# Optimization experiments

Hardware: AMD Instinct MI355X
Metric: run time of the kernel (lower is better)

The kernel has to match this reference:

```python
import jax, jax.numpy as jnp
import numpy as np

N, M, IN_DIM, OUT_DIM = 32768, 8192, 256, 64


def setup_inputs() -> dict:
    key = jax.random.key(0)
    k1, k2, k3, k4 = jax.random.split(key, 4)
    H = jax.random.bernoulli(k1, 0.01, (N, M)).astype(jnp.float32)
    w = jax.random.uniform(k2, (M,), minval=0.5, maxval=1.5, dtype=jnp.float32)
    x = jax.random.normal(k3, (N, IN_DIM), dtype=jnp.float32)
    W_lin = jax.random.normal(k4, (IN_DIM, OUT_DIM), dtype=jnp.float32) * (1.0 / np.sqrt(IN_DIM))
    b_lin = jnp.zeros((OUT_DIM,), dtype=jnp.float32)
    return {"x": x, "H": H, "w": w, "W_lin": W_lin, "b_lin": b_lin}


def reference(x, H, w, W_lin, b_lin):
    # Theta = Dv^{-1/2} H diag(w) De^{-1} H^T Dv^{-1/2}; out = Theta @ (x W + b).
    # Applied right-to-left with O(N) diagonal broadcasts instead of materializing
    # the [N, N] operator -- identical math to the torch reference.
    De = jnp.clip(jnp.sum(H, axis=0), 1.0, None)                 # [M] edge degrees
    Dv = jnp.clip(jnp.sum(H * w[None, :], axis=1), 1e-6, None)   # [N] weighted node degrees
    dv_inv_sqrt = Dv ** -0.5                                     # [N]
    y = x @ W_lin + b_lin                                        # [N, out]
    t = H.T @ (dv_inv_sqrt[:, None] * y)                         # [M, out] gather to edges
    t = (w / De)[:, None] * t                                    # edge scaling W De^{-1}
    out = dv_inv_sqrt[:, None] * (H @ t)                         # [N, out] scatter back
    return out
```

## Files before the change

kernel.cpp:

```cpp
#include <hip/hip_runtime.h>

#define N_NODES 32768
#define M_EDGES 8192
#define IN_DIM  256
#define OUT_F   64

#define SCAN_ROWS 16
#define NBLK   (N_NODES / SCAN_ROWS)
#define RBCAP  192
#define COLCAP 512

__global__ __launch_bounds__(256) void k_scan(const float* __restrict__ H,
                                              const float* __restrict__ w,
                                              unsigned short* __restrict__ rowidx,
                                              unsigned* __restrict__ rowlen,
                                              unsigned short* __restrict__ cscidx,
                                              unsigned* __restrict__ cscfill,
                                              float* __restrict__ Dv_raw) {
    int tid  = threadIdx.x;
    int lane = tid & 63;
    int wid  = tid >> 6;
    int row0 = blockIdx.x * SCAN_ROWS;

    for (int rr = wid; rr < SCAN_ROWS; rr += 4) {
        int n = row0 + rr;
        const float4* Hrow = (const float4*)(H + (size_t)n * M_EDGES);
        unsigned short* out_r = rowidx + (size_t)n * RBCAP;

        unsigned mreg[4];
        #pragma unroll
        for (int ob = 0; ob < 4; ++ob) {
            int jb = ob * 512;
            float4 h0 = Hrow[jb + lane];
            float4 h1 = Hrow[jb + 64  + lane];
            float4 h2 = Hrow[jb + 128 + lane];
            float4 h3 = Hrow[jb + 192 + lane];
            float4 h4 = Hrow[jb + 256 + lane];
            float4 h5 = Hrow[jb + 320 + lane];
            float4 h6 = Hrow[jb + 384 + lane];
            float4 h7 = Hrow[jb + 448 + lane];
            unsigned mk = 0;
            #define PK(hv, g)                                                  \
            {                                                                  \
                unsigned b = (unsigned)(hv.x != 0.f)                           \
                           | ((unsigned)(hv.y != 0.f) << 1)                    \
                           | ((unsigned)(hv.z != 0.f) << 2)                    \
                           | ((unsigned)(hv.w != 0.f) << 3);                   \
                mk |= b << (4 * (g));                                          \
            }
            PK(h0, 0) PK(h1, 1) PK(h2, 2) PK(h3, 3)
            PK(h4, 4) PK(h5, 5) PK(h6, 6) PK(h7, 7)
            #undef PK
            mreg[ob] = mk;
        }

        unsigned cnt = (unsigned)(__popc(mreg[0]) + __popc(mreg[1])
                                + __popc(mreg[2]) + __popc(mreg[3]));
        unsigned incl = cnt;
        #pragma unroll
        for (int off = 1; off < 64; off <<= 1) {
            unsigned v = (unsigned)__shfl_up((int)incl, off, 64);
            if (lane >= off) incl += v;
        }
        unsigned pos = incl - cnt;
        unsigned total = (unsigned)__shfl((int)incl, 63, 64);

        float dv = 0.f;
        #pragma unroll
        for (int r = 0; r < 4; ++r) {
            unsigned mm = mreg[r];
            while (mm) {
                int p = __ffs(mm) - 1;
                int g = p >> 2;
                int c4 = p & 3;
                int m_idx = r * 2048 + g * 256 + (lane << 2) + c4;
                if (pos < RBCAP) out_r[pos] = (unsigned short)m_idx;
                ++pos;
                dv += w[m_idx];
                unsigned fp = atomicAdd(&cscfill[m_idx], 1u);
                if (fp < (unsigned)COLCAP)
                    cscidx[(size_t)m_idx * COLCAP + fp] = (unsigned short)n;
                mm &= mm - 1;
            }
        }
        for (int off = 32; off; off >>= 1) dv += __shfl_down(dv, off, 64);
        if (lane == 0) Dv_raw[n] = dv;
        if (lane == 63)
            rowlen[n] = (total < (unsigned)RBCAP) ? total : (unsigned)RBCAP;
    }
}

__global__ __launch_bounds__(256) void k_lin(const float* __restrict__ x,
                                             const float* __restrict__ Wl,
                                             const float* __restrict__ b,
                                             const float* __restrict__ Dv_raw,
                                             float* __restrict__ y2) {
    __shared__ float x_s[16 * IN_DIM];
    int tid = threadIdx.x;
    int n0 = blockIdx.x * 16;
    for (int i = tid; i < 16 * IN_DIM; i += 256)
        x_s[i] = x[(size_t)n0 * IN_DIM + i];
    __syncthreads();
    int k = tid & 63;
    int rbase = tid >> 6;
    for (int pass = 0; pass < 4; ++pass) {
        int r = pass * 4 + rbase;
        float acc = b[k];
        const float* xr = x_s + r * IN_DIM;
        #pragma unroll 8
        for (int i = 0; i < IN_DIM; ++i)
            acc = fmaf(xr[i], Wl[i * OUT_F + k], acc);
        float dvis = rsqrtf(fmaxf(Dv_raw[n0 + r], 1e-6f));
        y2[(size_t)(n0 + r) * OUT_F + k] = acc * dvis;
    }
}

#define SEGQ(vi, base, cnt, src, ax, ay, az, aw, g, c, lane)                   \
if ((base) < (cnt)) {                                                          \
    unsigned rem = (cnt) - (base); if (rem > 64u) rem = 64u;                   \
    unsigned nq = (rem + 3u) >> 2;                                             \
    _Pragma("unroll 4")                                                        \
    for (unsigned qq = 0; qq < nq; ++qq) {                                     \
        int nidx = __shfl(vi, (int)(4u * qq) + (g), 64);                       \
        const float4* srcp = (const float4*)((src) + (size_t)nidx * OUT_F);    \
        float4 v = srcp[c];                                                    \
        bool ok = (4u * qq + (unsigned)(g)) < rem;                             \
        ax += ok ? v.x : 0.f;                                                  \
        ay += ok ? v.y : 0.f;                                                  \
        az += ok ? v.z : 0.f;                                                  \
        aw += ok ? v.w : 0.f;                                                  \
    }                                                                          \
}

__global__ __launch_bounds__(256) void k_edge(const unsigned short* __restrict__ cscidx,
                                              const unsigned* __restrict__ cscfill,
                                              const float* __restrict__ w,
                                              const float* __restrict__ y2,
                                              float* __restrict__ t) {
    int lane = threadIdx.x & 63;
    int wid  = threadIdx.x >> 6;
    int m = blockIdx.x * 4 + wid;
    unsigned de = cscfill[m];
    unsigned cnt = (de < (unsigned)COLCAP) ? de : (unsigned)COLCAP;
    const unsigned short* cp = cscidx + (size_t)m * COLCAP;
    int g = lane >> 4;
    int c = lane & 15;
    int v0 = cp[lane];         int v1 = cp[64  + lane];
    int v2 = cp[128 + lane];   int v3 = cp[192 + lane];
    int v4 = cp[256 + lane];   int v5 = cp[320 + lane];
    int v6 = cp[384 + lane];   int v7 = cp[448 + lane];
    float ax = 0.f, ay = 0.f, az = 0.f, aw = 0.f;
    SEGQ(v0,   0u, cnt, y2, ax, ay, az, aw, g, c, lane)
    SEGQ(v1,  64u, cnt, y2, ax, ay, az, aw, g, c, lane)
    SEGQ(v2, 128u, cnt, y2, ax, ay, az, aw, g, c, lane)
    SEGQ(v3, 192u, cnt, y2, ax, ay, az, aw, g, c, lane)
    SEGQ(v4, 256u, cnt, y2, ax, ay, az, aw, g, c, lane)
    SEGQ(v5, 320u, cnt, y2, ax, ay, az, aw, g, c, lane)
    SEGQ(v6, 384u, cnt, y2, ax, ay, az, aw, g, c, lane)
    SEGQ(v7, 448u, cnt, y2, ax, ay, az, aw, g, c, lane)
    ax += __shfl_xor(ax, 16, 64); ax += __shfl_xor(ax, 32, 64);
    ay += __shfl_xor(ay, 16, 64); ay += __shfl_xor(ay, 32, 64);
    az += __shfl_xor(az, 16, 64); az += __shfl_xor(az, 32, 64);
    aw += __shfl_xor(aw, 16, 64); aw += __shfl_xor(aw, 32, 64);
    if (g == 0) {
        float sc = w[m] / fmaxf((float)de, 1.0f);
        float4 r4 = { ax * sc, ay * sc, az * sc, aw * sc };
        ((float4*)(t + (size_t)m * OUT_F))[c] = r4;
    }
}

__global__ __launch_bounds__(256) void k_out(const unsigned short* __restrict__ rowidx,
                                             const unsigned* __restrict__ rowlen,
                                             const float* __restrict__ t,
                                             const float* __restrict__ Dv_raw,
                                             float* __restrict__ out) {
    int lane = threadIdx.x & 63;
    int wid  = threadIdx.x >> 6;
    int n = blockIdx.x * 4 + wid;
    unsigned cnt = rowlen[n];
    const unsigned short* rp = rowidx + (size_t)n * RBCAP;
    int g = lane >> 4;
    int c = lane & 15;
    int v0 = rp[lane];
    int v1 = rp[64  + lane];
    int v2 = rp[128 + lane];
    float ax = 0.f, ay = 0.f, az = 0.f, aw = 0.f;
    SEGQ(v0,   0u, cnt, t, ax, ay, az, aw, g, c, lane)
    SEGQ(v1,  64u, cnt, t, ax, ay, az, aw, g, c, lane)
    SEGQ(v2, 128u, cnt, t, ax, ay, az, aw, g, c, lane)
    ax += __shfl_xor(ax, 16, 64); ax += __shfl_xor(ax, 32, 64);
    ay += __shfl_xor(ay, 16, 64); ay += __shfl_xor(ay, 32, 64);
    az += __shfl_xor(az, 16, 64); az += __shfl_xor(az, 32, 64);
    aw += __shfl_xor(aw, 16, 64); aw += __shfl_xor(aw, 32, 64);
    if (g == 0) {
        float dvis = rsqrtf(fmaxf(Dv_raw[n], 1e-6f));
        float4 r4 = { ax * dvis, ay * dvis, az * dvis, aw * dvis };
        ((float4*)(out + (size_t)n * OUT_F))[c] = r4;
    }
}

extern "C" void kernel_launch(void* const* d_in, const int* in_sizes, int n_in,
                              void* d_out, int out_size, void* d_ws, size_t ws_size,
                              hipStream_t stream) {
    const float* x  = (const float*)d_in[0];
    const float* H  = (const float*)d_in[1];
    const float* w  = (const float*)d_in[2];
    const float* Wl = (const float*)d_in[3];
    const float* bl = (const float*)d_in[4];
    float* out = (float*)d_out;

    float*    y2      = (float*)d_ws;
    float*    t       = y2 + (size_t)N_NODES * OUT_F;
    float*    Dv_raw  = t + (size_t)M_EDGES * OUT_F;
    unsigned* rowlen  = (unsigned*)(Dv_raw + N_NODES);
    unsigned* cscfill = rowlen + N_NODES;
    unsigned short* rowidx = (unsigned short*)(cscfill + M_EDGES);
    unsigned short* cscidx = rowidx + (size_t)N_NODES * RBCAP;

    hipMemsetAsync(cscfill, 0, M_EDGES * sizeof(unsigned), stream);

    k_scan<<<dim3(NBLK),         dim3(256), 0, stream>>>(H, w, rowidx, rowlen, cscidx, cscfill, Dv_raw);
    k_lin <<<dim3(N_NODES / 16), dim3(256), 0, stream>>>(x, Wl, bl, Dv_raw, y2);
    k_edge<<<dim3(M_EDGES / 4),  dim3(256), 0, stream>>>(cscidx, cscfill, w, y2, t);
    k_out <<<dim3(N_NODES / 4),  dim3(256), 0, stream>>>(rowidx, rowlen, t, Dv_raw, out);
}
```

Before: 1.549 ms.

## Split CSC build out of scan, stage weights in LDS, split edge gather across waves

Moves the CSC transpose construction (atomics and scattered 16-bit stores) out of the H-streaming scan kernel into a separate kernel that reads the compact row index lists. The scan now sums w from a shared-memory copy. k_lin stages W_lin in LDS and uses two accumulators. k_edge assigns one edge per block, with four waves each handling 128 incidences, and reduces their partials through shared memory. The intent is to keep the dominant H read bandwidth-bound without atomic stalls, at the cost of an extra launch, the 64 KB w and W_lin LDS tiles limiting occupancy, and more k_edge blocks.

```diff
diff --git a/kernel.cpp b/kernel.cpp
--- a/kernel.cpp
+++ b/kernel.cpp
@@ -14,13 +14,16 @@
                                               const float* __restrict__ w,
                                               unsigned short* __restrict__ rowidx,
                                               unsigned* __restrict__ rowlen,
-                                              unsigned short* __restrict__ cscidx,
-                                              unsigned* __restrict__ cscfill,
                                               float* __restrict__ Dv_raw) {
+    __shared__ float w_s[M_EDGES];
     int tid  = threadIdx.x;
     int lane = tid & 63;
     int wid  = tid >> 6;
     int row0 = blockIdx.x * SCAN_ROWS;
+
+    for (int i = tid; i < M_EDGES / 4; i += 256)
+        ((float4*)w_s)[i] = ((const float4*)w)[i];
+    __syncthreads();
 
     for (int rr = wid; rr < SCAN_ROWS; rr += 4) {
         int n = row0 + rr;
@@ -76,10 +79,7 @@
                 int m_idx = r * 2048 + g * 256 + (lane << 2) + c4;
                 if (pos < RBCAP) out_r[pos] = (unsigned short)m_idx;
                 ++pos;
-                dv += w[m_idx];
-                unsigned fp = atomicAdd(&cscfill[m_idx], 1u);
-                if (fp < (unsigned)COLCAP)
-                    cscidx[(size_t)m_idx * COLCAP + fp] = (unsigned short)n;
+                dv += w_s[m_idx];
                 mm &= mm - 1;
             }
         }
@@ -87,6 +87,27 @@
         if (lane == 0) Dv_raw[n] = dv;
         if (lane == 63)
             rowlen[n] = (total < (unsigned)RBCAP) ? total : (unsigned)RBCAP;
+    }
+}
+
+__global__ __launch_bounds__(256) void k_csc(const unsigned short* __restrict__ rowidx,
+                                             const unsigned* __restrict__ rowlen,
+                                             unsigned short* __restrict__ cscidx,
+                                             unsigned* __restrict__ cscfill) {
+    int lane = threadIdx.x & 63;
+    int wid  = threadIdx.x >> 6;
+    int n = blockIdx.x * 4 + wid;
+    unsigned cnt = rowlen[n];
+    const unsigned short* rp = rowidx + (size_t)n * RBCAP;
+    #pragma unroll
+    for (int s = 0; s < 3; ++s) {
+        unsigned idx = (unsigned)(s * 64 + lane);
+        if (idx < cnt) {
+            int m = rp[idx];
+            unsigned fp = atomicAdd(&cscfill[m], 1u);
+            if (fp < (unsigned)COLCAP)
+                cscidx[(size_t)m * COLCAP + fp] = (unsigned short)n;
+        }
     }
 }
 
@@ -96,22 +117,27 @@
                                              const float* __restrict__ Dv_raw,
                                              float* __restrict__ y2) {
     __shared__ float x_s[16 * IN_DIM];
+    __shared__ float w_sh[IN_DIM * OUT_F];
     int tid = threadIdx.x;
     int n0 = blockIdx.x * 16;
-    for (int i = tid; i < 16 * IN_DIM; i += 256)
-        x_s[i] = x[(size_t)n0 * IN_DIM + i];
+    for (int i = tid; i < 16 * IN_DIM / 4; i += 256)
+        ((float4*)x_s)[i] = ((const float4*)(x + (size_t)n0 * IN_DIM))[i];
+    for (int i = tid; i < IN_DIM * OUT_F / 4; i += 256)
+        ((float4*)w_sh)[i] = ((const float4*)Wl)[i];
     __syncthreads();
     int k = tid & 63;
     int rbase = tid >> 6;
     for (int pass = 0; pass < 4; ++pass) {
         int r = pass * 4 + rbase;
-        float acc = b[k];
+        float acc0 = b[k], acc1 = 0.f;
         const float* xr = x_s + r * IN_DIM;
         #pragma unroll 8
-        for (int i = 0; i < IN_DIM; ++i)
-            acc = fmaf(xr[i], Wl[i * OUT_F + k], acc);
+        for (int i = 0; i < IN_DIM; i += 2) {
+            acc0 = fmaf(xr[i],     w_sh[i * OUT_F + k],       acc0);
+            acc1 = fmaf(xr[i + 1], w_sh[(i + 1) * OUT_F + k], acc1);
+        }
         float dvis = rsqrtf(fmaxf(Dv_raw[n0 + r], 1e-6f));
-        y2[(size_t)(n0 + r) * OUT_F + k] = acc * dvis;
+        y2[(size_t)(n0 + r) * OUT_F + k] = (acc0 + acc1) * dvis;
     }
 }
 
@@ -137,35 +163,36 @@
                                               const float* __restrict__ w,
                                               const float* __restrict__ y2,
                                               float* __restrict__ t) {
+    __shared__ float4 part[4 * 16];
     int lane = threadIdx.x & 63;
     int wid  = threadIdx.x >> 6;
-    int m = blockIdx.x * 4 + wid;
+    int m = blockIdx.x;
     unsigned de = cscfill[m];
     unsigned cnt = (de < (unsigned)COLCAP) ? de : (unsigned)COLCAP;
     const unsigned short* cp = cscidx + (size_t)m * COLCAP;
     int g = lane >> 4;
     int c = lane & 15;
-    int v0 = cp[lane];         int v1 = cp[64  + lane];
-    int v2 = cp[128 + lane];   int v3 = cp[192 + lane];
-    int v4 = cp[256 + lane];   int v5 = cp[320 + lane];
-    int v6 = cp[384 + lane];   int v7 = cp[448 + lane];
+    unsigned b0 = 128u * (unsigned)wid;
+    int v0 = cp[b0 + lane];
+    int v1 = cp[b0 + 64u + lane];
     float ax = 0.f, ay = 0.f, az = 0.f, aw = 0.f;
-    SEGQ(v0,   0u, cnt, y2, ax, ay, az, aw, g, c, lane)
-    SEGQ(v1,  64u, cnt, y2, ax, ay, az, aw, g, c, lane)
-    SEGQ(v2, 128u, cnt, y2, ax, ay, az, aw, g, c, lane)
-    SEGQ(v3, 192u, cnt, y2, ax, ay, az, aw, g, c, lane)
-    SEGQ(v4, 256u, cnt, y2, ax, ay, az, aw, g, c, lane)
-    SEGQ(v5, 320u, cnt, y2, ax, ay, az, aw, g, c, lane)
-    SEGQ(v6, 384u, cnt, y2, ax, ay, az, aw, g, c, lane)
-    SEGQ(v7, 448u, cnt, y2, ax, ay, az, aw, g, c, lane)
+    SEGQ(v0, b0,       cnt, y2, ax, ay, az, aw, g, c, lane)
+    SEGQ(v1, b0 + 64u, cnt, y2, ax, ay, az, aw, g, c, lane)
     ax += __shfl_xor(ax, 16, 64); ax += __shfl_xor(ax, 32, 64);
     ay += __shfl_xor(ay, 16, 64); ay += __shfl_xor(ay, 32, 64);
     az += __shfl_xor(az, 16, 64); az += __shfl_xor(az, 32, 64);
     aw += __shfl_xor(aw, 16, 64); aw += __shfl_xor(aw, 32, 64);
-    if (g == 0) {
+    if (g == 0) part[wid * 16 + c] = make_float4(ax, ay, az, aw);
+    __syncthreads();
+    if (threadIdx.x < 16) {
+        int cc = threadIdx.x;
+        float4 p0 = part[cc], p1 = part[16 + cc], p2 = part[32 + cc], p3 = part[48 + cc];
         float sc = w[m] / fmaxf((float)de, 1.0f);
-        float4 r4 = { ax * sc, ay * sc, az * sc, aw * sc };
-        ((float4*)(t + (size_t)m * OUT_F))[c] = r4;
+        float4 r4 = { (p0.x + p1.x + p2.x + p3.x) * sc,
+                      (p0.y + p1.y + p2.y + p3.y) * sc,
+                      (p0.z + p1.z + p2.z + p3.z) * sc,
+                      (p0.w + p1.w + p2.w + p3.w) * sc };
+        ((float4*)(t + (size_t)m * OUT_F))[cc] = r4;
     }
 }
 
@@ -219,8 +246,9 @@
 
     hipMemsetAsync(cscfill, 0, M_EDGES * sizeof(unsigned), stream);
 
-    k_scan<<<dim3(NBLK),         dim3(256), 0, stream>>>(H, w, rowidx, rowlen, cscidx, cscfill, Dv_raw);
+    k_scan<<<dim3(NBLK),         dim3(256), 0, stream>>>(H, w, rowidx, rowlen, Dv_raw);
+    k_csc <<<dim3(N_NODES / 4),  dim3(256), 0, stream>>>(rowidx, rowlen, cscidx, cscfill);
     k_lin <<<dim3(N_NODES / 16), dim3(256), 0, stream>>>(x, Wl, bl, Dv_raw, y2);
-    k_edge<<<dim3(M_EDGES / 4),  dim3(256), 0, stream>>>(cscidx, cscfill, w, y2, t);
+    k_edge<<<dim3(M_EDGES),      dim3(256), 0, stream>>>(cscidx, cscfill, w, y2, t);
     k_out <<<dim3(N_NODES / 4),  dim3(256), 0, stream>>>(rowidx, rowlen, t, Dv_raw, out);
 }
```

New measurement: 1.630 ms. +5.2%, slower.

## Replace sparse gather/scatter with dense bf16 MFMA GEMMs over H

Applied to the files above, without the earlier changes.

Swaps the sparse CSR/CSC build and gather kernels for dense matrix multiplies on the matrix cores. H is transposed into a bf16 copy for the H^T·z product, and H is packed to bf16 in registers for the H·t product. Activations are split into hi and lo bf16 halves to keep close to fp32 accuracy. Split-K partial sums are reduced in separate kernels. This removes the atomics and irregular gathers, but it reads all of dense H twice, writes a 512MB transposed copy, and does about 100x more arithmetic than the sparse path.

```diff
diff --git a/kernel.cpp b/kernel.cpp
--- a/kernel.cpp
+++ b/kernel.cpp
@@ -5,101 +5,78 @@
 #define IN_DIM  256
 #define OUT_F   64
 
-#define SCAN_ROWS 16
-#define NBLK   (N_NODES / SCAN_ROWS)
-#define RBCAP  192
-#define COLCAP 512
-
-__global__ __launch_bounds__(256) void k_scan(const float* __restrict__ H,
+#define KC1 16
+#define KC2 4
+
+typedef __attribute__((ext_vector_type(8))) short  bf16x8;
+typedef __attribute__((ext_vector_type(4))) float  f32x4;
+
+__device__ __forceinline__ unsigned short f2bf_rne(float f) {
+    unsigned u = __float_as_uint(f);
+    unsigned r = (u + 0x7FFFu + ((u >> 16) & 1u)) >> 16;
+    return (unsigned short)r;
+}
+__device__ __forceinline__ float bf2f(unsigned short h) {
+    return __uint_as_float(((unsigned)h) << 16);
+}
+
+__global__ __launch_bounds__(256) void k_prep(const float* __restrict__ H,
                                               const float* __restrict__ w,
-                                              unsigned short* __restrict__ rowidx,
-                                              unsigned* __restrict__ rowlen,
-                                              unsigned short* __restrict__ cscidx,
-                                              unsigned* __restrict__ cscfill,
-                                              float* __restrict__ Dv_raw) {
-    int tid  = threadIdx.x;
-    int lane = tid & 63;
-    int wid  = tid >> 6;
-    int row0 = blockIdx.x * SCAN_ROWS;
-
-    for (int rr = wid; rr < SCAN_ROWS; rr += 4) {
-        int n = row0 + rr;
-        const float4* Hrow = (const float4*)(H + (size_t)n * M_EDGES);
-        unsigned short* out_r = rowidx + (size_t)n * RBCAP;
-
-        unsigned mreg[4];
-        #pragma unroll
-        for (int ob = 0; ob < 4; ++ob) {
-            int jb = ob * 512;
-            float4 h0 = Hrow[jb + lane];
-            float4 h1 = Hrow[jb + 64  + lane];
-            float4 h2 = Hrow[jb + 128 + lane];
-            float4 h3 = Hrow[jb + 192 + lane];
-            float4 h4 = Hrow[jb + 256 + lane];
-            float4 h5 = Hrow[jb + 320 + lane];
-            float4 h6 = Hrow[jb + 384 + lane];
-            float4 h7 = Hrow[jb + 448 + lane];
-            unsigned mk = 0;
-            #define PK(hv, g)                                                  \
-            {                                                                  \
-                unsigned b = (unsigned)(hv.x != 0.f)                           \
-                           | ((unsigned)(hv.y != 0.f) << 1)                    \
-                           | ((unsigned)(hv.z != 0.f) << 2)                    \
-                           | ((unsigned)(hv.w != 0.f) << 3);                   \
-                mk |= b << (4 * (g));                                          \
-            }
-            PK(h0, 0) PK(h1, 1) PK(h2, 2) PK(h3, 3)
-            PK(h4, 4) PK(h5, 5) PK(h6, 6) PK(h7, 7)
-            #undef PK
-            mreg[ob] = mk;
-        }
-
-        unsigned cnt = (unsigned)(__popc(mreg[0]) + __popc(mreg[1])
-                                + __popc(mreg[2]) + __popc(mreg[3]));
-        unsigned incl = cnt;
-        #pragma unroll
-        for (int off = 1; off < 64; off <<= 1) {
-            unsigned v = (unsigned)__shfl_up((int)incl, off, 64);
-            if (lane >= off) incl += v;
-        }
-        unsigned pos = incl - cnt;
-        unsigned total = (unsigned)__shfl((int)incl, 63, 64);
-
-        float dv = 0.f;
-        #pragma unroll
-        for (int r = 0; r < 4; ++r) {
-            unsigned mm = mreg[r];
-            while (mm) {
-                int p = __ffs(mm) - 1;
-                int g = p >> 2;
-                int c4 = p & 3;
-                int m_idx = r * 2048 + g * 256 + (lane << 2) + c4;
-                if (pos < RBCAP) out_r[pos] = (unsigned short)m_idx;
-                ++pos;
-                dv += w[m_idx];
-                unsigned fp = atomicAdd(&cscfill[m_idx], 1u);
-                if (fp < (unsigned)COLCAP)
-                    cscidx[(size_t)m_idx * COLCAP + fp] = (unsigned short)n;
-                mm &= mm - 1;
-            }
-        }
-        for (int off = 32; off; off >>= 1) dv += __shfl_down(dv, off, 64);
-        if (lane == 0) Dv_raw[n] = dv;
-        if (lane == 63)
-            rowlen[n] = (total < (unsigned)RBCAP) ? total : (unsigned)RBCAP;
+                                              unsigned short* __restrict__ HT,
+                                              float* __restrict__ Dv_raw,
+                                              float* __restrict__ De) {
+    __shared__ unsigned short ht_s[128][264];
+    __shared__ float w_s[128];
+    __shared__ float de_s[128];
+    int t = threadIdx.x;
+    int n0 = blockIdx.x * 256;
+    int m0 = blockIdx.y * 128;
+    if (t < 128) { w_s[t] = w[m0 + t]; de_s[t] = 0.f; }
+    __syncthreads();
+
+    int c  = t & 31;
+    int rp = t >> 5;
+    float de0 = 0.f, de1 = 0.f, de2 = 0.f, de3 = 0.f;
+    for (int it = 0; it < 32; ++it) {
+        int r = it * 8 + rp;
+        float4 hv = ((const float4*)(H + (size_t)(n0 + r) * M_EDGES + m0))[c];
+        int mb = 4 * c;
+        ht_s[mb + 0][r] = (unsigned short)(__float_as_uint(hv.x) >> 16);
+        ht_s[mb + 1][r] = (unsigned short)(__float_as_uint(hv.y) >> 16);
+        ht_s[mb + 2][r] = (unsigned short)(__float_as_uint(hv.z) >> 16);
+        ht_s[mb + 3][r] = (unsigned short)(__float_as_uint(hv.w) >> 16);
+        float dp = hv.x * w_s[mb] + hv.y * w_s[mb + 1]
+                 + hv.z * w_s[mb + 2] + hv.w * w_s[mb + 3];
+        dp += __shfl_xor(dp, 1, 64);  dp += __shfl_xor(dp, 2, 64);
+        dp += __shfl_xor(dp, 4, 64);  dp += __shfl_xor(dp, 8, 64);
+        dp += __shfl_xor(dp, 16, 64);
+        if ((t & 31) == 0) atomicAdd(&Dv_raw[n0 + r], dp);
+        de0 += hv.x; de1 += hv.y; de2 += hv.z; de3 += hv.w;
+    }
+    atomicAdd(&de_s[4 * c + 0], de0);
+    atomicAdd(&de_s[4 * c + 1], de1);
+    atomicAdd(&de_s[4 * c + 2], de2);
+    atomicAdd(&de_s[4 * c + 3], de3);
+    __syncthreads();
+    if (t < 128) atomicAdd(&De[m0 + t], de_s[t]);
+
+    int lane = t & 63, wv = t >> 6;
+    for (int i = 0; i < 32; ++i) {
+        int ml = wv * 32 + i;
+        ushort4 v = *(const ushort4*)&ht_s[ml][lane * 4];
+        *(ushort4*)(HT + (size_t)(m0 + ml) * N_NODES + n0 + lane * 4) = v;
     }
 }
 
 __global__ __launch_bounds__(256) void k_lin(const float* __restrict__ x,
                                              const float* __restrict__ Wl,
                                              const float* __restrict__ b,
-                                             const float* __restrict__ Dv_raw,
-                                             float* __restrict__ y2) {
+                                             float* __restrict__ y) {
     __shared__ float x_s[16 * IN_DIM];
     int tid = threadIdx.x;
     int n0 = blockIdx.x * 16;
-    for (int i = tid; i < 16 * IN_DIM; i += 256)
-        x_s[i] = x[(size_t)n0 * IN_DIM + i];
+    for (int i = tid; i < 16 * IN_DIM / 4; i += 256)
+        ((float4*)x_s)[i] = ((const float4*)(x + (size_t)n0 * IN_DIM))[i];
     __syncthreads();
     int k = tid & 63;
     int rbase = tid >> 6;
@@ -110,93 +87,205 @@
         #pragma unroll 8
         for (int i = 0; i < IN_DIM; ++i)
             acc = fmaf(xr[i], Wl[i * OUT_F + k], acc);
-        float dvis = rsqrtf(fmaxf(Dv_raw[n0 + r], 1e-6f));
-        y2[(size_t)(n0 + r) * OUT_F + k] = acc * dvis;
-    }
-}
-
-#define SEGQ(vi, base, cnt, src, ax, ay, az, aw, g, c, lane)                   \
-if ((base) < (cnt)) {                                                          \
-    unsigned rem = (cnt) - (base); if (rem > 64u) rem = 64u;                   \
-    unsigned nq = (rem + 3u) >> 2;                                             \
-    _Pragma("unroll 4")                                                        \
-    for (unsigned qq = 0; qq < nq; ++qq) {                                     \
-        int nidx = __shfl(vi, (int)(4u * qq) + (g), 64);                       \
-        const float4* srcp = (const float4*)((src) + (size_t)nidx * OUT_F);    \
-        float4 v = srcp[c];                                                    \
-        bool ok = (4u * qq + (unsigned)(g)) < rem;                             \
-        ax += ok ? v.x : 0.f;                                                  \
-        ay += ok ? v.y : 0.f;                                                  \
-        az += ok ? v.z : 0.f;                                                  \
-        aw += ok ? v.w : 0.f;                                                  \
-    }                                                                          \
-}
-
-__global__ __launch_bounds__(256) void k_edge(const unsigned short* __restrict__ cscidx,
-                                              const unsigned* __restrict__ cscfill,
-                                              const float* __restrict__ w,
-                                              const float* __restrict__ y2,
-                                              float* __restrict__ t) {
-    int lane = threadIdx.x & 63;
-    int wid  = threadIdx.x >> 6;
-    int m = blockIdx.x * 4 + wid;
-    unsigned de = cscfill[m];
-    unsigned cnt = (de < (unsigned)COLCAP) ? de : (unsigned)COLCAP;
-    const unsigned short* cp = cscidx + (size_t)m * COLCAP;
-    int g = lane >> 4;
-    int c = lane & 15;
-    int v0 = cp[lane];         int v1 = cp[64  + lane];
-    int v2 = cp[128 + lane];   int v3 = cp[192 + lane];
-    int v4 = cp[256 + lane];   int v5 = cp[320 + lane];
-    int v6 = cp[384 + lane];   int v7 = cp[448 + lane];
-    float ax = 0.f, ay = 0.f, az = 0.f, aw = 0.f;
-    SEGQ(v0,   0u, cnt, y2, ax, ay, az, aw, g, c, lane)
-    SEGQ(v1,  64u, cnt, y2, ax, ay, az, aw, g, c, lane)
-    SEGQ(v2, 128u, cnt, y2, ax, ay, az, aw, g, c, lane)
-    SEGQ(v3, 192u, cnt, y2, ax, ay, az, aw, g, c, lane)
-    SEGQ(v4, 256u, cnt, y2, ax, ay, az, aw, g, c, lane)
-    SEGQ(v5, 320u, cnt, y2, ax, ay, az, aw, g, c, lane)
-    SEGQ(v6, 384u, cnt, y2, ax, ay, az, aw, g, c, lane)
-    SEGQ(v7, 448u, cnt, y2, ax, ay, az, aw, g, c, lane)
-    ax += __shfl_xor(ax, 16, 64); ax += __shfl_xor(ax, 32, 64);
-    ay += __shfl_xor(ay, 16, 64); ay += __shfl_xor(ay, 32, 64);
-    az += __shfl_xor(az, 16, 64); az += __shfl_xor(az, 32, 64);
-    aw += __shfl_xor(aw, 16, 64); aw += __shfl_xor(aw, 32, 64);
-    if (g == 0) {
-        float sc = w[m] / fmaxf((float)de, 1.0f);
-        float4 r4 = { ax * sc, ay * sc, az * sc, aw * sc };
-        ((float4*)(t + (size_t)m * OUT_F))[c] = r4;
-    }
-}
-
-__global__ __launch_bounds__(256) void k_out(const unsigned short* __restrict__ rowidx,
-                                             const unsigned* __restrict__ rowlen,
-                                             const float* __restrict__ t,
+        y[(size_t)(n0 + r) * OUT_F + k] = acc;
+    }
+}
+
+__global__ __launch_bounds__(256) void k_zt(const float* __restrict__ y,
+                                            const float* __restrict__ Dv_raw,
+                                            unsigned short* __restrict__ zTh,
+                                            unsigned short* __restrict__ zTl) {
+    __shared__ unsigned short zh_s[64][264];
+    __shared__ unsigned short zl_s[64][264];
+    __shared__ float dvis_s[256];
+    int t = threadIdx.x;
+    int n0 = blockIdx.x * 256;
+    dvis_s[t] = rsqrtf(fmaxf(Dv_raw[n0 + t], 1e-6f));
+    __syncthreads();
+    int c = t & 15, rp = t >> 4;
+    for (int it = 0; it < 16; ++it) {
+        int r = it * 16 + rp;
+        float4 v = ((const float4*)(y + (size_t)(n0 + r) * OUT_F))[c];
+        float dvs = dvis_s[r];
+        float zv[4] = { v.x * dvs, v.y * dvs, v.z * dvs, v.w * dvs };
+        #pragma unroll
+        for (int j = 0; j < 4; ++j) {
+            unsigned short hi = f2bf_rne(zv[j]);
+            float lo = zv[j] - bf2f(hi);
+            zh_s[4 * c + j][r] = hi;
+            zl_s[4 * c + j][r] = f2bf_rne(lo);
+        }
+    }
+    __syncthreads();
+    int lane = t & 63, wv = t >> 6;
+    for (int i = 0; i < 16; ++i) {
+        int kk = wv * 16 + i;
+        *(ushort4*)(zTh + (size_t)kk * N_NODES + n0 + lane * 4) =
+            *(const ushort4*)&zh_s[kk][lane * 4];
+        *(ushort4*)(zTl + (size_t)kk * N_NODES + n0 + lane * 4) =
+            *(const ushort4*)&zl_s[kk][lane * 4];
+    }
+}
+
+__global__ __launch_bounds__(256) void g1(const unsigned short* __restrict__ HT,
+                                          const unsigned short* __restrict__ zTh,
+                                          const unsigned short* __restrict__ zTl,
+                                          float* __restrict__ t_part) {
+    int t = threadIdx.x;
+    int lane = t & 63, wv = t >> 6;
+    int l15 = lane & 15, l4 = lane >> 4;
+    int m_base = blockIdx.x * 256 + wv * 64;
+    int kc = blockIdx.y;
+    int k_base = kc * (N_NODES / KC1);
+
+    f32x4 acc[4][4];
+    #pragma unroll
+    for (int i = 0; i < 4; ++i)
+        #pragma unroll
+        for (int j = 0; j < 4; ++j) acc[i][j] = (f32x4){0.f, 0.f, 0.f, 0.f};
+
+    for (int kk = 0; kk < N_NODES / KC1; kk += 32) {
+        int kidx = k_base + kk + l4 * 8;
+        bf16x8 a[4], bh[4], bl[4];
+        #pragma unroll
+        for (int fr = 0; fr < 4; ++fr)
+            a[fr] = *(const bf16x8*)(HT + (size_t)(m_base + fr * 16 + l15) * N_NODES + kidx);
+        #pragma unroll
+        for (int fc = 0; fc < 4; ++fc) {
+            bh[fc] = *(const bf16x8*)(zTh + (size_t)(fc * 16 + l15) * N_NODES + kidx);
+            bl[fc] = *(const bf16x8*)(zTl + (size_t)(fc * 16 + l15) * N_NODES + kidx);
+        }
+        #pragma unroll
+        for (int fr = 0; fr < 4; ++fr)
+            #pragma unroll
+            for (int fc = 0; fc < 4; ++fc) {
+                acc[fr][fc] = __builtin_amdgcn_mfma_f32_16x16x32_bf16(a[fr], bh[fc], acc[fr][fc], 0, 0, 0);
+                acc[fr][fc] = __builtin_amdgcn_mfma_f32_16x16x32_bf16(a[fr], bl[fc], acc[fr][fc], 0, 0, 0);
+            }
+    }
+    float* dst = t_part + (size_t)kc * M_EDGES * OUT_F;
+    #pragma unroll
+    for (int fr = 0; fr < 4; ++fr)
+        #pragma unroll
+        for (int fc = 0; fc < 4; ++fc)
+            #pragma unroll
+            for (int r = 0; r < 4; ++r) {
+                int row = m_base + fr * 16 + l4 * 4 + r;
+                int col = fc * 16 + l15;
+                dst[(size_t)row * OUT_F + col] = acc[fr][fc][r];
+            }
+}
+
+__global__ __launch_bounds__(256) void k_tt(const float* __restrict__ t_part,
+                                            const float* __restrict__ w,
+                                            const float* __restrict__ De,
+                                            unsigned short* __restrict__ tTh,
+                                            unsigned short* __restrict__ tTl) {
+    __shared__ unsigned short th_s[64][136];
+    __shared__ unsigned short tl_s[64][136];
+    int t = threadIdx.x;
+    int m0 = blockIdx.x * 128;
+    int c = t & 15, rr = t >> 4;
+    for (int it = 0; it < 8; ++it) {
+        int ml = it * 16 + rr;
+        float4 s = {0.f, 0.f, 0.f, 0.f};
+        #pragma unroll
+        for (int kc = 0; kc < KC1; ++kc) {
+            float4 v = ((const float4*)(t_part + ((size_t)kc * M_EDGES + m0 + ml) * OUT_F))[c];
+            s.x += v.x; s.y += v.y; s.z += v.z; s.w += v.w;
+        }
+        float sc = w[m0 + ml] / fmaxf(De[m0 + ml], 1.0f);
+        float sv[4] = { s.x * sc, s.y * sc, s.z * sc, s.w * sc };
+        #pragma unroll
+        for (int j = 0; j < 4; ++j) {
+            unsigned short hi = f2bf_rne(sv[j]);
+            th_s[4 * c + j][ml] = hi;
+            tl_s[4 * c + j][ml] = f2bf_rne(sv[j] - bf2f(hi));
+        }
+    }
+    __syncthreads();
+    int lane = t & 63, wv = t >> 6;
+    for (int i = 0; i < 16; ++i) {
+        int kk = wv * 16 + i;
+        *(ushort2*)(tTh + (size_t)kk * M_EDGES + m0 + lane * 2) =
+            *(const ushort2*)&th_s[kk][lane * 2];
+        *(ushort2*)(tTl + (size_t)kk * M_EDGES + m0 + lane * 2) =
+            *(const ushort2*)&tl_s[kk][lane * 2];
+    }
+}
+
+__global__ __launch_bounds__(256) void g2(const float* __restrict__ H,
+                                          const unsigned short* __restrict__ tTh,
+                                          const unsigned short* __restrict__ tTl,
+                                          float* __restrict__ out_part) {
+    int t = threadIdx.x;
+    int lane = t & 63, wv = t >> 6;
+    int l15 = lane & 15, l4 = lane >> 4;
+    int n_base = blockIdx.x * 256 + wv * 64;
+    int h = blockIdx.y;
+    int k_base = h * (M_EDGES / KC2);
+
+    f32x4 acc[4][4];
+    #pragma unroll
+    for (int i = 0; i < 4; ++i)
+        #pragma unroll
+        for (int j = 0; j < 4; ++j) acc[i][j] = (f32x4){0.f, 0.f, 0.f, 0.f};
+
+    for (int kk = 0; kk < M_EDGES / KC2; kk += 32) {
+        int kidx = k_base + kk + l4 * 8;
+        bf16x8 a[4], bh[4], bl[4];
+        #pragma unroll
+        for (int fr = 0; fr < 4; ++fr) {
+            const float* hp = H + (size_t)(n_base + fr * 16 + l15) * M_EDGES + kidx;
+            float4 q0 = *(const float4*)hp;
+            float4 q1 = *(const float4*)(hp + 4);
+            union { unsigned u[4]; bf16x8 v; } pk;
+            pk.u[0] = __builtin_amdgcn_perm(__float_as_uint(q0.y), __float_as_uint(q0.x), 0x07060302u);
+            pk.u[1] = __builtin_amdgcn_perm(__float_as_uint(q0.w), __float_as_uint(q0.z), 0x07060302u);
+            pk.u[2] = __builtin_amdgcn_perm(__float_as_uint(q1.y), __float_as_uint(q1.x), 0x07060302u);
+            pk.u[3] = __builtin_amdgcn_perm(__float_as_uint(q1.w), __float_as_uint(q1.z), 0x07060302u);
+            a[fr] = pk.v;
+        }
+        #pragma unroll
+        for (int fc = 0; fc < 4; ++fc) {
+            bh[fc] = *(const bf16x8*)(tTh + (size_t)(fc * 16 + l15) * M_EDGES + kidx);
+            bl[fc] = *(const bf16x8*)(tTl + (size_t)(fc * 16 + l15) * M_EDGES + kidx);
+        }
+        #pragma unroll
+        for (int fr = 0; fr < 4; ++fr)
+            #pragma unroll
+            for (int fc = 0; fc < 4; ++fc) {
+                acc[fr][fc] = __builtin_amdgcn_mfma_f32_16x16x32_bf16(a[fr], bh[fc], acc[fr][fc], 0, 0, 0);
+                acc[fr][fc] = __builtin_amdgcn_mfma_f32_16x16x32_bf16(a[fr], bl[fc], acc[fr][fc], 0, 0, 0);
+            }
+    }
+    float* dst = out_part + (size_t)h * N_NODES * OUT_F;
+    #pragma unroll
+    for (int fr = 0; fr < 4; ++fr)
+        #pragma unroll
+        for (int fc = 0; fc < 4; ++fc)
+            #pragma unroll
+            for (int r = 0; r < 4; ++r) {
+                int row = n_base + fr * 16 + l4 * 4 + r;
+                int col = fc * 16 + l15;
+                dst[(size_t)row * OUT_F + col] = acc[fr][fc][r];
+            }
+}
+
+__global__ __launch_bounds__(256) void k_fin(const float* __restrict__ out_part,
                                              const float* __restrict__ Dv_raw,
                                              float* __restrict__ out) {
-    int lane = threadIdx.x & 63;
-    int wid  = threadIdx.x >> 6;
-    int n = blockIdx.x * 4 + wid;
-    unsigned cnt = rowlen[n];
-    const unsigned short* rp = rowidx + (size_t)n * RBCAP;
-    int g = lane >> 4;
-    int c = lane & 15;
-    int v0 = rp[lane];
-    int v1 = rp[64  + lane];
-    int v2 = rp[128 + lane];
-    float ax = 0.f, ay = 0.f, az = 0.f, aw = 0.f;
-    SEGQ(v0,   0u, cnt, t, ax, ay, az, aw, g, c, lane)
-    SEGQ(v1,  64u, cnt, t, ax, ay, az, aw, g, c, lane)
-    SEGQ(v2, 128u, cnt, t, ax, ay, az, aw, g, c, lane)
-    ax += __shfl_xor(ax, 16, 64); ax += __shfl_xor(ax, 32, 64);
-    ay += __shfl_xor(ay, 16, 64); ay += __shfl_xor(ay, 32, 64);
-    az += __shfl_xor(az, 16, 64); az += __shfl_xor(az, 32, 64);
-    aw += __shfl_xor(aw, 16, 64); aw += __shfl_xor(aw, 32, 64);
-    if (g == 0) {
-        float dvis = rsqrtf(fmaxf(Dv_raw[n], 1e-6f));
-        float4 r4 = { ax * dvis, ay * dvis, az * dvis, aw * dvis };
-        ((float4*)(out + (size_t)n * OUT_F))[c] = r4;
-    }
+    int i4 = blockIdx.x * 256 + threadIdx.x;
+    int n = i4 >> 4;
+    float4 s = {0.f, 0.f, 0.f, 0.f};
+    #pragma unroll
+    for (int h = 0; h < KC2; ++h) {
+        float4 v = ((const float4*)(out_part + (size_t)h * N_NODES * OUT_F))[i4];
+        s.x += v.x; s.y += v.y; s.z += v.z; s.w += v.w;
+    }
+    float dvis = rsqrtf(fmaxf(Dv_raw[n], 1e-6f));
+    float4 r = { s.x * dvis, s.y * dvis, s.z * dvis, s.w * dvis };
+    ((float4*)out)[i4] = r;
 }
 
 extern "C" void kernel_launch(void* const* d_in, const int* in_sizes, int n_in,
@@ -209,18 +298,24 @@
     const float* bl = (const float*)d_in[4];
     float* out = (float*)d_out;
 
-    float*    y2      = (float*)d_ws;
-    float*    t       = y2 + (size_t)N_NODES * OUT_F;
-    float*    Dv_raw  = t + (size_t)M_EDGES * OUT_F;
-    unsigned* rowlen  = (unsigned*)(Dv_raw + N_NODES);
-    unsigned* cscfill = rowlen + N_NODES;
-    unsigned short* rowidx = (unsigned short*)(cscfill + M_EDGES);
-    unsigned short* cscidx = rowidx + (size_t)N_NODES * RBCAP;
-
-    hipMemsetAsync(cscfill, 0, M_EDGES * sizeof(unsigned), stream);
-
-    k_scan<<<dim3(NBLK),         dim3(256), 0, stream>>>(H, w, rowidx, rowlen, cscidx, cscfill, Dv_raw);
-    k_lin <<<dim3(N_NODES / 16), dim3(256), 0, stream>>>(x, Wl, bl, Dv_raw, y2);
-    k_edge<<<dim3(M_EDGES / 4),  dim3(256), 0, stream>>>(cscidx, cscfill, w, y2, t);
-    k_out <<<dim3(N_NODES / 4),  dim3(256), 0, stream>>>(rowidx, rowlen, t, Dv_raw, out);
-}
+    float* y      = (float*)d_ws;
+    float* Dv_raw = y + (size_t)N_NODES * OUT_F;
+    float* De     = Dv_raw + N_NODES;
+    float* t_part = De + M_EDGES;
+    float* o_part = t_part + (size_t)KC1 * M_EDGES * OUT_F;
+    unsigned short* HT  = (unsigned short*)(o_part + (size_t)KC2 * N_NODES * OUT_F);
+    unsigned short* zTh = HT + (size_t)M_EDGES * N_NODES;
+    unsigned short* zTl = zTh + (size_t)OUT_F * N_NODES;
+    unsigned short* tTh = zTl + (size_t)OUT_F * N_NODES;
+    unsigned short* tTl = tTh + (size_t)OUT_F * M_EDGES;
+
+    hipMemsetAsync(Dv_raw, 0, (N_NODES + M_EDGES) * sizeof(float), stream);
+
+    k_prep<<<dim3(N_NODES / 256, M_EDGES / 128), dim3(256), 0, stream>>>(H, w, HT, Dv_raw, De);
+    k_lin <<<dim3(N_NODES / 16),                 dim3(256), 0, stream>>>(x, Wl, bl, y);
+    k_zt  <<<dim3(N_NODES / 256),                dim3(256), 0, stream>>>(y, Dv_raw, zTh, zTl);
+    g1    <<<dim3(M_EDGES / 256, KC1),           dim3(256), 0, stream>>>(HT, zTh, zTl, t_part);
+    k_tt  <<<dim3(M_EDGES / 128),                dim3(256), 0, stream>>>(t_part, w, De, tTh, tTl);
+    g2    <<<dim3(N_NODES / 256, KC2),           dim3(256), 0, stream>>>(H, tTh, tTl, o_part);
+    k_fin <<<dim3(N_NODES * OUT_F / 4 / 256),    dim3(256), 0, stream>>>(o_part, Dv_raw, out);
+}
```

After: 2.322 ms. 49.9% more time.
